# Kernel optimization log

Hardware: AMD Instinct MI355X
Metric: run time of the kernel (lower is better)

The kernel has to match this reference:

```python
import jax, jax.numpy as jnp
import numpy as np

N_NODES = 50000
N_EDGES = 800000
NODE_DIM = 27
HIDDEN = 64
CTX = 32
HEADS = 4
NEG_SLOPE = 0.2


def _gat_layer(x, src, dst, W, a_src, a_dst, bias, n_nodes):
    # x: [N, F_in], W: [F_in, H*C], a_src/a_dst: [H, C], bias: [C]
    h = (x @ W).reshape(n_nodes, HEADS, -1)            # [N, H, C]
    alpha_src = jnp.einsum('nhc,hc->nh', h, a_src)     # [N, H]
    alpha_dst = jnp.einsum('nhc,hc->nh', h, a_dst)     # [N, H]
    e = alpha_src[src] + alpha_dst[dst]                # [E, H]
    e = jax.nn.leaky_relu(e, NEG_SLOPE)
    # segment softmax over edges grouped by destination node
    e_max = jax.ops.segment_max(e, dst, num_segments=n_nodes)  # [N, H]
    e_exp = jnp.exp(e - e_max[dst])                    # [E, H]
    denom = jax.ops.segment_sum(e_exp, dst, num_segments=n_nodes)  # [N, H]
    alpha = e_exp / denom[dst]                         # [E, H]
    msg = alpha[:, :, None] * h[src]                   # [E, H, C]
    out = jax.ops.segment_sum(msg, dst, num_segments=n_nodes)      # [N, H, C]
    return out.mean(axis=1) + bias                     # concat=False -> head mean


def setup_inputs() -> dict:
    key = jax.random.key(0)
    ks = jax.random.split(key, 16)
    glorot = lambda k, shp: jax.random.normal(k, shp, jnp.float32) * jnp.sqrt(2.0 / (shp[0] + shp[-1]))
    inp = {
        'x': jax.random.normal(ks[0], (N_NODES, NODE_DIM), jnp.float32),
        'edge_index': jax.random.randint(ks[1], (2, N_EDGES), 0, N_NODES, jnp.int32),
        'donor_emb': jax.random.normal(ks[2], (1, CTX), jnp.float32),
        # GAT layer 1
        'W1': glorot(ks[3], (NODE_DIM, HEADS * HIDDEN)),
        'a_src1': glorot(ks[4], (HEADS, HIDDEN)),
        'a_dst1': glorot(ks[5], (HEADS, HIDDEN)),
        'b1': jnp.zeros((HIDDEN,), jnp.float32),
        # GAT layer 2
        'W2': glorot(ks[6], (HIDDEN, HEADS * HIDDEN)),
        'a_src2': glorot(ks[7], (HEADS, HIDDEN)),
        'a_dst2': glorot(ks[8], (HEADS, HIDDEN)),
        'b2': jnp.zeros((HIDDEN,), jnp.float32),
        # scorer MLP
        'Ws1': glorot(ks[9], (HIDDEN + CTX, HIDDEN)),
        'bs1': jnp.zeros((HIDDEN,), jnp.float32),
        'Ws2': glorot(ks[10], (HIDDEN, 1)),
        'bs2': jnp.zeros((1,), jnp.float32),
    }
    return inp


def reference(x, edge_index, donor_emb, W1, a_src1, a_dst1, b1,
              W2, a_src2, a_dst2, b2, Ws1, bs1, Ws2, bs2):
    n = x.shape[0]
    # PyG GATConv default add_self_loops=True
    loop = jnp.arange(n, dtype=edge_index.dtype)
    src = jnp.concatenate([edge_index[0], loop])
    dst = jnp.concatenate([edge_index[1], loop])

    h = jax.nn.elu(_gat_layer(x, src, dst, W1, a_src1, a_dst1, b1, n))
    h = jax.nn.elu(_gat_layer(h, src, dst, W2, a_src2, a_dst2, b2, n))

    ctx = jnp.concatenate([h, jnp.broadcast_to(donor_emb, (n, donor_emb.shape[-1]))], axis=-1)
    hidden = jax.nn.relu(ctx @ Ws1 + bs1)
    logits = (hidden @ Ws2 + bs2).squeeze(-1)          # [N]
    return logits
```

## Files before the change

### kernel.cpp

```cpp
#include <hip/hip_runtime.h>
#include <hip/hip_fp16.h>
#include <cmath>

#define NEG 0.2f

typedef __attribute__((ext_vector_type(8))) short short8;
typedef __attribute__((ext_vector_type(4))) float f32x4;
typedef __fp16 half2_t __attribute__((ext_vector_type(2)));

__device__ __forceinline__ float leaky(float v){ return v > 0.f ? v : NEG * v; }

__device__ __forceinline__ short bf16_rne(float f){
    unsigned u = __float_as_uint(f);
    unsigned r = u + 0x7fffu + ((u >> 16) & 1u);
    return (short)(r >> 16);
}
__device__ __forceinline__ float bf16_to_f(short s){
    return __uint_as_float(((unsigned)(unsigned short)s) << 16);
}
__device__ __forceinline__ half2_t bc16(unsigned u){ return __builtin_bit_cast(half2_t, u); }
__device__ __forceinline__ unsigned packh2(float a, float b){
    __half ha = __float2half(a), hb = __float2half(b);
    return (unsigned)__builtin_bit_cast(unsigned short, ha)
         | ((unsigned)__builtin_bit_cast(unsigned short, hb) << 16);
}

__device__ __forceinline__ int block_excl_scan(int v, int* ws4){
    int tid = threadIdx.x, lane = tid & 63, wv = tid >> 6;
    int incl = v;
    #pragma unroll
    for (int off = 1; off < 64; off <<= 1){
        int t = __shfl_up(incl, off);
        if (lane >= off) incl += t;
    }
    if (lane == 63) ws4[wv] = incl;
    __syncthreads();
    int add = 0;
    for (int w = 0; w < wv; ++w) add += ws4[w];
    return incl - v + add;
}


__global__ __launch_bounds__(256) void prep_hist_kernel(
    const float* __restrict__ W1, const float* __restrict__ W2,
    const float* __restrict__ Ws1, const float* __restrict__ bs1,
    const float* __restrict__ donor,
    const float* __restrict__ as1, const float* __restrict__ ad1,
    const float* __restrict__ as2, const float* __restrict__ ad2,
    short* __restrict__ w1p, short* __restrict__ w2p,
    short* __restrict__ s1hi, short* __restrict__ s1lo, float* __restrict__ d1p,
    float* __restrict__ hat1s, float* __restrict__ hat1d,
    float* __restrict__ hat2s, float* __restrict__ hat2d,
    const int* __restrict__ ei, int E, int N, int NB, int* __restrict__ bucket_cnt)
{
    if ((int)blockIdx.x < 256){
        int t = blockIdx.x * 256 + threadIdx.x;
        int T = 256 * 256;
        for (int i = t; i < 64 * 136; i += T){
            int c = i / 136, kk = i % 136; short v = 0;
            if (kk < 128){ int h = kk >> 5, k = kk & 31;
                if (k < 27) v = bf16_rne(W1[(size_t)k * 256 + h * 64 + c] * 0.25f); }
            w1p[i] = v;
        }
        for (int i = t; i < 64 * 264; i += T){
            int c = i / 264, kk = i % 264; short v = 0;
            if (kk < 256){ int h = kk >> 6, k = kk & 63;
                v = bf16_rne(W2[(size_t)k * 256 + h * 64 + c] * 0.25f); }
            w2p[i] = v;
        }
        for (int i = t; i < 64 * 72; i += T){
            int nn = i / 72, k = i % 72;
            float v = (k < 64) ? Ws1[(size_t)k * 64 + nn] : 0.f;
            short hi = bf16_rne(v);
            s1hi[i] = hi; s1lo[i] = bf16_rne(v - bf16_to_f(hi));
        }
        if (t < 64){
            float s = bs1[t];
            for (int k = 0; k < 32; ++k) s = fmaf(donor[k], Ws1[(size_t)(64 + k) * 64 + t], s);
            d1p[t] = s;
        }
        if (t < 128){
            int h = t >> 5, k = t & 31;
            float s = 0.f, d = 0.f;
            if (k < 27)
                for (int c = 0; c < 64; ++c){
                    float w = W1[(size_t)k * 256 + h * 64 + c];
                    s = fmaf(w, as1[h * 64 + c], s);
                    d = fmaf(w, ad1[h * 64 + c], d);
                }
            hat1s[t] = s; hat1d[t] = d;
        }
        if (t < 256){
            int h = t >> 6, k = t & 63;
            float s = 0.f, d = 0.f;
            for (int c = 0; c < 64; ++c){
                float w = W2[(size_t)k * 256 + h * 64 + c];
                s = fmaf(w, as2[h * 64 + c], s);
                d = fmaf(w, ad2[h * 64 + c], d);
            }
            hat2s[t] = s; hat2d[t] = d;
        }
    } else {
        __shared__ int lh[256];
        int tid = threadIdx.x;
        int ET = E + N;
        int ebase = ((int)blockIdx.x - 256) * 2048;
        lh[tid] = 0;
        __syncthreads();
        #pragma unroll
        for (int j = 0; j < 8; ++j){
            int e = ebase + j * 256 + tid;
            if (e < ET){
                int d = (e < E) ? ei[E + e] : (e - E);
                atomicAdd(&lh[d >> 8], 1);
            }
        }
        __syncthreads();
        if (tid < NB && lh[tid]) atomicAdd(&bucket_cnt[tid], lh[tid]);
    }
}


__global__ __launch_bounds__(256) void coarse_scatter_kernel(
    const int* __restrict__ ei, int E, int N, int NB,
    const int* __restrict__ bucket_cnt, int* __restrict__ bucket_cursor,
    unsigned* __restrict__ pairs)
{
    __shared__ int ws4[4];
    __shared__ int gbase[256];
    __shared__ int lh[256];
    __shared__ int gb[256];
    int tid = threadIdx.x;
    int ET = E + N;
    {
        int v = (tid < NB) ? bucket_cnt[tid] : 0;
        gbase[tid] = block_excl_scan(v, ws4);
    }
    lh[tid] = 0;
    __syncthreads();
    int ebase = blockIdx.x * 2048;
    int d[8], s[8], r[8];
    #pragma unroll
    for (int j = 0; j < 8; ++j){
        int e = ebase + j * 256 + tid;
        d[j] = -1;
        if (e < ET){
            if (e < E){ s[j] = ei[e]; d[j] = ei[E + e]; } else { s[j] = d[j] = e - E; }
            r[j] = atomicAdd(&lh[d[j] >> 8], 1);
        }
    }
    __syncthreads();
    if (tid < NB && lh[tid]) gb[tid] = gbase[tid] + atomicAdd(&bucket_cursor[tid], lh[tid]);
    __syncthreads();
    #pragma unroll
    for (int j = 0; j < 8; ++j){
        if (d[j] >= 0)
            pairs[gb[d[j] >> 8] + r[j]] = ((unsigned)d[j] << 16) | (unsigned)s[j];
    }
}


__device__ __forceinline__ void fine_sort_body(
    int b, const unsigned* __restrict__ pairs, const int* __restrict__ bucket_cnt, int NB,
    int* __restrict__ colsrc, int* __restrict__ rowptr, int N, int ET)
{
    __shared__ int ws4f[4];
    __shared__ int sb[257];
    __shared__ int hist[256];
    __shared__ int cur[256];
    int tid = threadIdx.x;
    {
        int v = (tid < NB) ? bucket_cnt[tid] : 0;
        int excl = block_excl_scan(v, ws4f);
        sb[tid] = excl;
        if (tid == 255) sb[256] = excl + v;
    }
    hist[tid] = 0;
    __syncthreads();
    int base = sb[b], endb = sb[b + 1];
    int cnt = endb - base;
    int d0 = b << 8;
    for (int i = tid; i < cnt; i += 256){
        unsigned p = pairs[base + i];
        atomicAdd(&hist[(int)(p >> 16) - d0], 1);
    }
    __syncthreads();
    int v = hist[tid];
    int excl = block_excl_scan(v, ws4f);
    cur[tid] = excl;
    if (d0 + tid < N) rowptr[d0 + tid] = base + excl;
    if (b == 0 && tid == 0) rowptr[N] = ET;
    __syncthreads();
    for (int i = tid; i < cnt; i += 256){
        unsigned p = pairs[base + i];
        int r = atomicAdd(&cur[(int)(p >> 16) - d0], 1);
        colsrc[base + r] = (int)(p & 0xFFFFu);
    }
}


__global__ __launch_bounds__(256) void xprep_fine_kernel(
    const float* __restrict__ x, const float* __restrict__ hat1s, const float* __restrict__ hat1d,
    float* __restrict__ xp, float* __restrict__ asrc, float* __restrict__ adst, int N,
    int XB, const unsigned* __restrict__ pairs, const int* __restrict__ bucket_cnt, int NB,
    int* __restrict__ colsrc, int* __restrict__ rowptr, int ET)
{
    if ((int)blockIdx.x < XB){
        int t0 = blockIdx.x * 256 + threadIdx.x, T = XB * 256;
        for (int i = t0; i < N * 32; i += T){
            int nn = i >> 5, k = i & 31;
            xp[i] = (k < 27) ? x[(size_t)nn * 27 + k] : 0.f;
        }
        for (int nn = t0; nn < N; nn += T){
            float xr[27];
            #pragma unroll
            for (int k = 0; k < 27; ++k) xr[k] = x[(size_t)nn * 27 + k];
            #pragma unroll
            for (int h = 0; h < 4; ++h){
                float s = 0.f, d = 0.f;
                #pragma unroll
                for (int k = 0; k < 27; ++k){
                    s = fmaf(xr[k], hat1s[h * 32 + k], s);
                    d = fmaf(xr[k], hat1d[h * 32 + k], d);
                }
                asrc[nn * 4 + h] = s;
                adst[nn * 4 + h] = d;
            }
        }
    } else {
        fine_sort_body(blockIdx.x - XB, pairs, bucket_cnt, NB, colsrc, rowptr, N, ET);
    }
}


template<int L>
__device__ __forceinline__ void agg_edge(const char* __restrict__ pay, int boff, int o,
    unsigned aw, unsigned bw, float* accx, float* accy)
{
    half2_t ah = bc16(aw), bh = bc16(bw);
    float w0 = (float)ah[0], w1 = (float)ah[1], w2 = (float)bh[0], w3 = (float)bh[1];
    if (L == 1){
        float xv = *(const float*)(pay + o + boff);
        accx[0] = fmaf(w0, xv, accx[0]);
        accx[1] = fmaf(w1, xv, accx[1]);
        accx[2] = fmaf(w2, xv, accx[2]);
        accx[3] = fmaf(w3, xv, accx[3]);
    } else {
        unsigned hv = *(const unsigned*)(pay + o + boff);
        half2_t hh = bc16(hv);
        float c0 = (float)hh[0], c1 = (float)hh[1];
        accx[0] = fmaf(w0, c0, accx[0]); accy[0] = fmaf(w0, c1, accy[0]);
        accx[1] = fmaf(w1, c0, accx[1]); accy[1] = fmaf(w1, c1, accy[1]);
        accx[2] = fmaf(w2, c0, accx[2]); accy[2] = fmaf(w2, c1, accy[2]);
        accx[3] = fmaf(w3, c0, accx[3]); accy[3] = fmaf(w3, c1, accy[3]);
    }
}

template<int L>
__global__ __launch_bounds__(256) void aggregate_kernel(
    const int* __restrict__ rowptr, const int* __restrict__ colsrc,
    const char* __restrict__ pay, const float* __restrict__ asrc,
    const float* __restrict__ adst, char* __restrict__ gout, int N)
{
    int tid = threadIdx.x;
    int grp = tid >> 5;
    int lane32 = tid & 31;
    int n = blockIdx.x * 8 + grp;
    if (n >= N) return;
    int start = rowptr[n], end = rowptr[n + 1];
    int deg = end - start;
    const float4 ad = *(const float4*)(adst + (size_t)n * 4);

    int src0 = 0;
    float e0 = -1e30f, e1 = -1e30f, e2 = -1e30f, e3 = -1e30f;
    bool v0 = lane32 < deg;
    if (v0){
        src0 = colsrc[start + lane32];
        float4 as = *(const float4*)(asrc + (size_t)src0 * 4);
        e0 = leaky(as.x + ad.x); e1 = leaky(as.y + ad.y);
        e2 = leaky(as.z + ad.z); e3 = leaky(as.w + ad.w);
    }

    float m0, m1, m2, m3, i0, i1, i2, i3, p0, p1, p2, p3;
    if (deg <= 32){
        m0 = e0; m1 = e1; m2 = e2; m3 = e3;
        #pragma unroll
        for (int off = 1; off < 32; off <<= 1){
            m0 = fmaxf(m0, __shfl_xor(m0, off));
            m1 = fmaxf(m1, __shfl_xor(m1, off));
            m2 = fmaxf(m2, __shfl_xor(m2, off));
            m3 = fmaxf(m3, __shfl_xor(m3, off));
        }
        p0 = __expf(e0 - m0);
        p1 = __expf(e1 - m1);
        p2 = __expf(e2 - m2);
        p3 = __expf(e3 - m3);
        float t0 = p0, t1 = p1, t2 = p2, t3 = p3;
        #pragma unroll
        for (int off = 1; off < 32; off <<= 1){
            t0 += __shfl_xor(t0, off);
            t1 += __shfl_xor(t1, off);
            t2 += __shfl_xor(t2, off);
            t3 += __shfl_xor(t3, off);
        }
        i0 = 1.f / t0; i1 = 1.f / t1; i2 = 1.f / t2; i3 = 1.f / t3;
    } else {
        m0 = e0; m1 = e1; m2 = e2; m3 = e3;
        float t0 = v0 ? 1.f : 0.f, t1 = t0, t2 = t0, t3 = t0;
        for (int i = start + 32 + lane32; i < end; i += 32){
            int s = colsrc[i];
            float4 as = *(const float4*)(asrc + (size_t)s * 4);
            float e, nm;
            e = leaky(as.x + ad.x); nm = fmaxf(m0, e); t0 = t0 * __expf(m0 - nm) + __expf(e - nm); m0 = nm;
            e = leaky(as.y + ad.y); nm = fmaxf(m1, e); t1 = t1 * __expf(m1 - nm) + __expf(e - nm); m1 = nm;
            e = leaky(as.z + ad.z); nm = fmaxf(m2, e); t2 = t2 * __expf(m2 - nm) + __expf(e - nm); m2 = nm;
            e = leaky(as.w + ad.w); nm = fmaxf(m3, e); t3 = t3 * __expf(m3 - nm) + __expf(e - nm); m3 = nm;
        }
        #pragma unroll
        for (int off = 1; off < 32; off <<= 1){
            float om, os, nm;
            om = __shfl_xor(m0, off); os = __shfl_xor(t0, off);
            nm = fmaxf(m0, om); t0 = t0 * __expf(m0 - nm) + os * __expf(om - nm); m0 = nm;
            om = __shfl_xor(m1, off); os = __shfl_xor(t1, off);
            nm = fmaxf(m1, om); t1 = t1 * __expf(m1 - nm) + os * __expf(om - nm); m1 = nm;
            om = __shfl_xor(m2, off); os = __shfl_xor(t2, off);
            nm = fmaxf(m2, om); t2 = t2 * __expf(m2 - nm) + os * __expf(om - nm); m2 = nm;
            om = __shfl_xor(m3, off); os = __shfl_xor(t3, off);
            nm = fmaxf(m3, om); t3 = t3 * __expf(m3 - nm) + os * __expf(om - nm); m3 = nm;
        }
        i0 = 1.f / t0; i1 = 1.f / t1; i2 = 1.f / t2; i3 = 1.f / t3;
        p0 = __expf(e0 - m0); p1 = __expf(e1 - m1);
        p2 = __expf(e2 - m2); p3 = __expf(e3 - m3);
    }

    float accx[4] = {0.f, 0.f, 0.f, 0.f};
    float accy[4] = {0.f, 0.f, 0.f, 0.f};
    const int boff = lane32 * 4;
    bool first = true;
    for (int base = start; base < end; base += 32){
        int cnt = end - base; if (cnt > 32) cnt = 32;
        float w0, w1, w2, w3; int off = 0;
        if (first){
            w0 = p0 * i0; w1 = p1 * i1; w2 = p2 * i2; w3 = p3 * i3;
            off = v0 ? src0 * 128 : 0;
        } else {
            w0 = w1 = w2 = w3 = 0.f;
            if (lane32 < cnt){
                int s = colsrc[base + lane32];
                float4 as = *(const float4*)(asrc + (size_t)s * 4);
                w0 = __expf(leaky(as.x + ad.x) - m0) * i0;
                w1 = __expf(leaky(as.y + ad.y) - m1) * i1;
                w2 = __expf(leaky(as.z + ad.z) - m2) * i2;
                w3 = __expf(leaky(as.w + ad.w) - m3) * i3;
                off = s * 128;
            }
        }
        first = false;
        half2_t q01 = __builtin_amdgcn_cvt_pkrtz(w0, w1);
        half2_t q23 = __builtin_amdgcn_cvt_pkrtz(w2, w3);
        int wx = (int)__builtin_bit_cast(unsigned, q01);
        int wy = (int)__builtin_bit_cast(unsigned, q23);

        int j = 0;
        for (; j + 2 <= cnt; j += 2){
            int o0 = __shfl(off, j, 32);
            unsigned a0 = (unsigned)__shfl(wx, j, 32), b0 = (unsigned)__shfl(wy, j, 32);
            int o1 = __shfl(off, j + 1, 32);
            unsigned a1 = (unsigned)__shfl(wx, j + 1, 32), b1 = (unsigned)__shfl(wy, j + 1, 32);
            agg_edge<L>(pay, boff, o0, a0, b0, accx, accy);
            agg_edge<L>(pay, boff, o1, a1, b1, accx, accy);
        }
        for (; j < cnt; ++j){
            int o0 = __shfl(off, j, 32);
            unsigned a0 = (unsigned)__shfl(wx, j, 32), b0 = (unsigned)__shfl(wy, j, 32);
            agg_edge<L>(pay, boff, o0, a0, b0, accx, accy);
        }
    }

    if (L == 1){
        float* g = (float*)gout;
        #pragma unroll
        for (int h = 0; h < 4; ++h)
            g[(size_t)n * 128 + h * 32 + lane32] = accx[h];
    } else {
        #pragma unroll
        for (int h = 0; h < 4; ++h){
            unsigned u = packh2(accx[h], accy[h]);
            *(unsigned*)(gout + (size_t)n * 512 + h * 128 + lane32 * 4) = u;
        }
    }
}


__global__ __launch_bounds__(256) void t1post_kernel(
    const float* __restrict__ G1, const short* __restrict__ w1p, const float* __restrict__ b1,
    const float* __restrict__ hat2s, const float* __restrict__ hat2d,
    __half* __restrict__ hm16, float* __restrict__ asrc, float* __restrict__ adst, int N)
{
    constexpr int WP = 136;
    __shared__ short wt[64 * WP];
    const int tid = threadIdx.x;
    const int n0 = blockIdx.x * 64;
    const int wv = tid >> 6, lane = tid & 63;
    const int quad = lane >> 4, ln = lane & 15;
    const int myrow = wv * 16 + ln;
    const int nme = n0 + myrow;

    {
        const short8* g = (const short8*)w1p;
        short8* l = (short8*)wt;
        for (int t = tid; t < 64 * WP / 8; t += 256) l[t] = g[t];
    }
    __syncthreads();

    f32x4 acc[4];
    #pragma unroll
    for (int i = 0; i < 4; ++i) acc[i] = (f32x4){0.f, 0.f, 0.f, 0.f};

    #pragma unroll
    for (int ks = 0; ks < 4; ++ks){
        const int k0 = ks * 32 + quad * 8;
        float4 f0 = make_float4(0.f, 0.f, 0.f, 0.f), f1 = f0;
        if (nme < N){
            const float* ap = G1 + (size_t)nme * 128 + k0;
            f0 = *(const float4*)ap;
            f1 = *(const float4*)(ap + 4);
        }
        float fa[8] = {f0.x, f0.y, f0.z, f0.w, f1.x, f1.y, f1.z, f1.w};
        short8 ahi, alo;
        #pragma unroll
        for (int e = 0; e < 8; ++e){
            short hi = bf16_rne(fa[e]);
            ahi[e] = hi;
            alo[e] = bf16_rne(fa[e] - bf16_to_f(hi));
        }
        #pragma unroll
        for (int nt = 0; nt < 4; ++nt){
            short8 bhi = *(const short8*)(wt + (nt * 16 + ln) * WP + k0);
            acc[nt] = __builtin_amdgcn_mfma_f32_16x16x32_bf16(ahi, bhi, acc[nt], 0, 0, 0);
            acc[nt] = __builtin_amdgcn_mfma_f32_16x16x32_bf16(alo, bhi, acc[nt], 0, 0, 0);
        }
    }

    float b1v[4], hs[4][4], hd[4][4];
    #pragma unroll
    for (int nt = 0; nt < 4; ++nt) b1v[nt] = b1[nt * 16 + ln];
    #pragma unroll
    for (int h = 0; h < 4; ++h)
        #pragma unroll
        for (int nt = 0; nt < 4; ++nt){
            hs[h][nt] = hat2s[h * 64 + nt * 16 + ln];
            hd[h][nt] = hat2d[h * 64 + nt * 16 + ln];
        }

    #pragma unroll
    for (int r = 0; r < 4; ++r){
        int n = n0 + wv * 16 + quad * 4 + r;
        float ev[4];
        #pragma unroll
        for (int nt = 0; nt < 4; ++nt){
            float v = acc[nt][r] + b1v[nt];
            v = (v > 0.f) ? v : expm1f(v);
            ev[nt] = v;
        }
        if (n < N){
            #pragma unroll
            for (int nt = 0; nt < 4; ++nt)
                hm16[(size_t)n * 64 + nt * 16 + ln] = __float2half(ev[nt]);
        }
        #pragma unroll
        for (int h = 0; h < 4; ++h){
            float ps = 0.f, pd = 0.f;
            #pragma unroll
            for (int nt = 0; nt < 4; ++nt){
                ps = fmaf(ev[nt], hs[h][nt], ps);
                pd = fmaf(ev[nt], hd[h][nt], pd);
            }
            #pragma unroll
            for (int off = 1; off < 16; off <<= 1){
                ps += __shfl_xor(ps, off);
                pd += __shfl_xor(pd, off);
            }
            if (ln == 0 && n < N){
                asrc[n * 4 + h] = ps;
                adst[n * 4 + h] = pd;
            }
        }
    }
}


__global__ __launch_bounds__(256) void t2post_kernel(
    const char* __restrict__ G2, const short* __restrict__ w2p, const float* __restrict__ b2,
    float* __restrict__ hmid2, int N)
{
    constexpr int WP = 264;
    __shared__ short wt[64 * WP];
    const int tid = threadIdx.x;
    const int n0 = blockIdx.x * 64;
    const int wv = tid >> 6, lane = tid & 63;
    const int quad = lane >> 4, ln = lane & 15;
    const int myrow = wv * 16 + ln;
    const int nme = n0 + myrow;

    {
        const short8* g = (const short8*)w2p;
        short8* l = (short8*)wt;
        for (int t = tid; t < 64 * WP / 8; t += 256) l[t] = g[t];
    }
    __syncthreads();

    f32x4 acc[4];
    #pragma unroll
    for (int i = 0; i < 4; ++i) acc[i] = (f32x4){0.f, 0.f, 0.f, 0.f};

    #pragma unroll
    for (int ks = 0; ks < 8; ++ks){
        const int k0 = ks * 32 + quad * 8;
        uint4 u = make_uint4(0u, 0u, 0u, 0u);
        if (nme < N)
            u = *(const uint4*)(G2 + (size_t)nme * 512 + (size_t)k0 * 2);
        half2_t h0 = bc16(u.x), h1 = bc16(u.y), h2 = bc16(u.z), h3 = bc16(u.w);
        float fa[8] = {(float)h0[0], (float)h0[1], (float)h1[0], (float)h1[1],
                       (float)h2[0], (float)h2[1], (float)h3[0], (float)h3[1]};
        short8 ahi, alo;
        #pragma unroll
        for (int e = 0; e < 8; ++e){
            short hi = bf16_rne(fa[e]);
            ahi[e] = hi;
            alo[e] = bf16_rne(fa[e] - bf16_to_f(hi));
        }
        #pragma unroll
        for (int nt = 0; nt < 4; ++nt){
            short8 bhi = *(const short8*)(wt + (nt * 16 + ln) * WP + k0);
            acc[nt] = __builtin_amdgcn_mfma_f32_16x16x32_bf16(ahi, bhi, acc[nt], 0, 0, 0);
            acc[nt] = __builtin_amdgcn_mfma_f32_16x16x32_bf16(alo, bhi, acc[nt], 0, 0, 0);
        }
    }

    float b2v[4];
    #pragma unroll
    for (int nt = 0; nt < 4; ++nt) b2v[nt] = b2[nt * 16 + ln];
    #pragma unroll
    for (int r = 0; r < 4; ++r){
        int n = n0 + wv * 16 + quad * 4 + r;
        if (n < N){
            #pragma unroll
            for (int nt = 0; nt < 4; ++nt){
                float v = acc[nt][r] + b2v[nt];
                v = (v > 0.f) ? v : expm1f(v);
                hmid2[(size_t)n * 64 + nt * 16 + ln] = v;
            }
        }
    }
}


__global__ __launch_bounds__(256) void scorer_mfma_kernel(
    const float* __restrict__ h2, const short* __restrict__ s1hi, const short* __restrict__ s1lo,
    const float* __restrict__ d1p, const float* __restrict__ Ws2, const float* __restrict__ bs2,
    float* __restrict__ out, int N)
{
    constexpr int WP = 72;
    __shared__ short whi[64 * WP];
    __shared__ short wlo[64 * WP];
    const int tid = threadIdx.x;
    const int n0 = blockIdx.x * 64;

    const int wv = tid >> 6, lane = tid & 63;
    const int quad = lane >> 4, ln = lane & 15;
    const int myrow = wv * 16 + ln;
    const int nme = n0 + myrow;

    float fdir[16];
    #pragma unroll
    for (int ks = 0; ks < 2; ++ks){
        float4 f0 = make_float4(0.f, 0.f, 0.f, 0.f), f1 = f0;
        if (nme < N){
            const float* ap = h2 + (size_t)nme * 64 + ks * 32 + quad * 8;
            f0 = *(const float4*)ap;
            f1 = *(const float4*)(ap + 4);
        }
        fdir[ks*8+0]=f0.x; fdir[ks*8+1]=f0.y; fdir[ks*8+2]=f0.z; fdir[ks*8+3]=f0.w;
        fdir[ks*8+4]=f1.x; fdir[ks*8+5]=f1.y; fdir[ks*8+6]=f1.z; fdir[ks*8+7]=f1.w;
    }
    {
        const short8* ghi = (const short8*)s1hi;
        const short8* glo = (const short8*)s1lo;
        short8* lhi = (short8*)whi;
        short8* llo = (short8*)wlo;
        for (int t = tid; t < 64 * WP / 8; t += 256){ lhi[t] = ghi[t]; llo[t] = glo[t]; }
    }
    __syncthreads();

    f32x4 acc[4];
    #pragma unroll
    for (int i = 0; i < 4; ++i) acc[i] = (f32x4){0.f, 0.f, 0.f, 0.f};

    #pragma unroll
    for (int ks = 0; ks < 2; ++ks) {
        const int k0 = ks * 32 + quad * 8;
        short8 ahi, alo;
        #pragma unroll
        for (int e = 0; e < 8; ++e) {
            float v = fdir[ks * 8 + e];
            short hi = bf16_rne(v);
            ahi[e] = hi;
            alo[e] = bf16_rne(v - bf16_to_f(hi));
        }
        #pragma unroll
        for (int nt = 0; nt < 4; ++nt) {
            short8 bhi = *(const short8*)(whi + (nt * 16 + ln) * WP + k0);
            short8 blo = *(const short8*)(wlo + (nt * 16 + ln) * WP + k0);
            acc[nt] = __builtin_amdgcn_mfma_f32_16x16x32_bf16(ahi, bhi, acc[nt], 0, 0, 0);
            acc[nt] = __builtin_amdgcn_mfma_f32_16x16x32_bf16(alo, bhi, acc[nt], 0, 0, 0);
            acc[nt] = __builtin_amdgcn_mfma_f32_16x16x32_bf16(ahi, blo, acc[nt], 0, 0, 0);
        }
    }

    float d1v[4], w2v[4];
    #pragma unroll
    for (int nt = 0; nt < 4; ++nt){
        d1v[nt] = d1p[nt * 16 + ln];
        w2v[nt] = Ws2[nt * 16 + ln];
    }
    float b2 = bs2[0];
    #pragma unroll
    for (int r = 0; r < 4; ++r){
        float t = 0.f;
        #pragma unroll
        for (int nt = 0; nt < 4; ++nt)
            t = fmaf(fmaxf(acc[nt][r] + d1v[nt], 0.f), w2v[nt], t);
        #pragma unroll
        for (int off = 1; off < 16; off <<= 1) t += __shfl_xor(t, off);
        if (ln == 0){
            int n = n0 + wv * 16 + quad * 4 + r;
            if (n < N) out[n] = t + b2;
        }
    }
}


extern "C" void kernel_launch(void* const* d_in, const int* in_sizes, int n_in,
                              void* d_out, int out_size, void* d_ws, size_t ws_size,
                              hipStream_t stream)
{
    const float* x    = (const float*)d_in[0];
    const int*   ei   = (const int*)  d_in[1];
    const float* donor= (const float*)d_in[2];
    const float* W1   = (const float*)d_in[3];
    const float* as1  = (const float*)d_in[4];
    const float* ad1  = (const float*)d_in[5];
    const float* b1   = (const float*)d_in[6];
    const float* W2   = (const float*)d_in[7];
    const float* as2  = (const float*)d_in[8];
    const float* ad2  = (const float*)d_in[9];
    const float* b2   = (const float*)d_in[10];
    const float* Ws1  = (const float*)d_in[11];
    const float* bs1  = (const float*)d_in[12];
    const float* Ws2  = (const float*)d_in[13];
    const float* bs2  = (const float*)d_in[14];

    const int N  = in_sizes[0] / 27;
    const int E  = in_sizes[1] / 2;
    const int ET = E + N;
    const int NB = (N + 255) / 256;

    char* ws = (char*)d_ws;
    auto alloc = [&](size_t bytes) -> void* {
        void* p = (void*)ws;
        ws += (bytes + 255) / 256 * 256;
        return p;
    };
    int*      rowptr  = (int*)     alloc((size_t)(N + 1) * 4);
    int*      colsrc  = (int*)     alloc((size_t)ET * 4);
    unsigned* pairs   = (unsigned*)alloc((size_t)ET * 4);
    float*    xp      = (float*)   alloc((size_t)N * 128);
    char*     gbuf    = (char*)    alloc((size_t)N * 512);
    __half*   hm16    = (__half*)  alloc((size_t)N * 128);
    float*    hmid2   = (float*)   alloc((size_t)N * 256);
    float*    asrc    = (float*)   alloc((size_t)N * 4 * 4);
    float*    adst    = (float*)   alloc((size_t)N * 4 * 4);
    int*      bucket_cnt    = (int*) alloc(256 * 4);
    int*      bucket_cursor = (int*) alloc(256 * 4);
    short*    w1p     = (short*)   alloc(64 * 136 * 2);
    short*    w2p     = (short*)   alloc(64 * 264 * 2);
    short*    s1hi    = (short*)   alloc(64 * 72 * 2);
    short*    s1lo    = (short*)   alloc(64 * 72 * 2);
    float*    d1p     = (float*)   alloc(64 * 4);
    float*    hat1s   = (float*)   alloc(128 * 4);
    float*    hat1d   = (float*)   alloc(128 * 4);
    float*    hat2s   = (float*)   alloc(256 * 4);
    float*    hat2d   = (float*)   alloc(256 * 4);

    const int nblk = (N + 63) / 64;
    const int hblk = (ET + 2047) / 2048;
    const int XB   = 512;

    (void)hipMemsetAsync(bucket_cnt, 0, 512 * 4, stream);
    prep_hist_kernel<<<256 + hblk, 256, 0, stream>>>(
        W1, W2, Ws1, bs1, donor, as1, ad1, as2, ad2,
        w1p, w2p, s1hi, s1lo, d1p, hat1s, hat1d, hat2s, hat2d,
        ei, E, N, NB, bucket_cnt);
    coarse_scatter_kernel<<<hblk, 256, 0, stream>>>(ei, E, N, NB, bucket_cnt, bucket_cursor, pairs);
    xprep_fine_kernel<<<XB + NB, 256, 0, stream>>>(
        x, hat1s, hat1d, xp, asrc, adst, N,
        XB, pairs, bucket_cnt, NB, colsrc, rowptr, ET);
    aggregate_kernel<1><<<(N + 7) / 8, 256, 0, stream>>>(
        rowptr, colsrc, (const char*)xp, asrc, adst, gbuf, N);
    t1post_kernel<<<nblk, 256, 0, stream>>>(
        (const float*)gbuf, w1p, b1, hat2s, hat2d, hm16, asrc, adst, N);
    aggregate_kernel<2><<<(N + 7) / 8, 256, 0, stream>>>(
        rowptr, colsrc, (const char*)hm16, asrc, adst, gbuf, N);
    t2post_kernel<<<nblk, 256, 0, stream>>>(
        (const char*)gbuf, w2p, b2, hmid2, N);
    scorer_mfma_kernel<<<nblk, 256, 0, stream>>>(
        hmid2, s1hi, s1lo, d1p, Ws2, bs2, (float*)d_out, N);
}
```

Before: 233.3 us.

## Fuse t2post with scorer, move x prep into prep kernel, store x as fp16

The t2post and scorer kernels become one kernel that keeps the layer-2 output in shared memory, so the fp32 hmid2 round trip through global memory and one launch go away. The x padding and layer-1 attention-logit computation move into the prep/histogram kernel, which now computes hat1 per block in shared memory. The fine sort becomes its own kernel. The padded x is stored as fp16, and layer-1 aggregation reads half2 with two edges per pass across half-warps, halving gather bytes at some cost in input precision.

```diff
diff --git a/kernel.cpp b/kernel.cpp
--- a/kernel.cpp
+++ b/kernel.cpp
@@ -47,14 +47,17 @@
     const float* __restrict__ donor,
     const float* __restrict__ as1, const float* __restrict__ ad1,
     const float* __restrict__ as2, const float* __restrict__ ad2,
+    const float* __restrict__ x,
     short* __restrict__ w1p, short* __restrict__ w2p,
     short* __restrict__ s1hi, short* __restrict__ s1lo, float* __restrict__ d1p,
-    float* __restrict__ hat1s, float* __restrict__ hat1d,
     float* __restrict__ hat2s, float* __restrict__ hat2d,
-    const int* __restrict__ ei, int E, int N, int NB, int* __restrict__ bucket_cnt)
+    __half* __restrict__ xp, float* __restrict__ asrc, float* __restrict__ adst,
+    const int* __restrict__ ei, int E, int N, int NB, int* __restrict__ bucket_cnt,
+    int hblk, int XBP)
 {
-    if ((int)blockIdx.x < 256){
-        int t = blockIdx.x * 256 + threadIdx.x;
+    int b = (int)blockIdx.x;
+    if (b < 256){
+        int t = b * 256 + threadIdx.x;
         int T = 256 * 256;
         for (int i = t; i < 64 * 136; i += T){
             int c = i / 136, kk = i % 136; short v = 0;
@@ -79,8 +82,38 @@
             for (int k = 0; k < 32; ++k) s = fmaf(donor[k], Ws1[(size_t)(64 + k) * 64 + t], s);
             d1p[t] = s;
         }
-        if (t < 128){
-            int h = t >> 5, k = t & 31;
+        if (t < 256){
+            int h = t >> 6, k = t & 63;
+            float s = 0.f, d = 0.f;
+            for (int c = 0; c < 64; ++c){
+                float w = W2[(size_t)k * 256 + h * 64 + c];
+                s = fmaf(w, as2[h * 64 + c], s);
+                d = fmaf(w, ad2[h * 64 + c], d);
+            }
+            hat2s[t] = s; hat2d[t] = d;
+        }
+    } else if (b < 256 + hblk){
+        __shared__ int lh[256];
+        int tid = threadIdx.x;
+        int ET = E + N;
+        int ebase = (b - 256) * 2048;
+        lh[tid] = 0;
+        __syncthreads();
+        #pragma unroll
+        for (int j = 0; j < 8; ++j){
+            int e = ebase + j * 256 + tid;
+            if (e < ET){
+                int d = (e < E) ? ei[E + e] : (e - E);
+                atomicAdd(&lh[d >> 8], 1);
+            }
+        }
+        __syncthreads();
+        if (tid < NB && lh[tid]) atomicAdd(&bucket_cnt[tid], lh[tid]);
+    } else {
+        __shared__ float h1s[128], h1d[128];
+        int tid = threadIdx.x;
+        if (tid < 128){
+            int h = tid >> 5, k = tid & 31;
             float s = 0.f, d = 0.f;
             if (k < 27)
                 for (int c = 0; c < 64; ++c){
@@ -88,35 +121,31 @@
                     s = fmaf(w, as1[h * 64 + c], s);
                     d = fmaf(w, ad1[h * 64 + c], d);
                 }
-            hat1s[t] = s; hat1d[t] = d;
-        }
-        if (t < 256){
-            int h = t >> 6, k = t & 63;
-            float s = 0.f, d = 0.f;
-            for (int c = 0; c < 64; ++c){
-                float w = W2[(size_t)k * 256 + h * 64 + c];
-                s = fmaf(w, as2[h * 64 + c], s);
-                d = fmaf(w, ad2[h * 64 + c], d);
-            }
-            hat2s[t] = s; hat2d[t] = d;
-        }
-    } else {
-        __shared__ int lh[256];
-        int tid = threadIdx.x;
-        int ET = E + N;
-        int ebase = ((int)blockIdx.x - 256) * 2048;
-        lh[tid] = 0;
+            h1s[tid] = s; h1d[tid] = d;
+        }
         __syncthreads();
-        #pragma unroll
-        for (int j = 0; j < 8; ++j){
-            int e = ebase + j * 256 + tid;
-            if (e < ET){
-                int d = (e < E) ? ei[E + e] : (e - E);
-                atomicAdd(&lh[d >> 8], 1);
-            }
-        }
-        __syncthreads();
-        if (tid < NB && lh[tid]) atomicAdd(&bucket_cnt[tid], lh[tid]);
+        int pb = b - 256 - hblk;
+        int t0 = pb * 256 + tid, T = XBP * 256;
+        for (int i = t0; i < N * 32; i += T){
+            int nn = i >> 5, k = i & 31;
+            xp[i] = __float2half((k < 27) ? x[(size_t)nn * 27 + k] : 0.f);
+        }
+        for (int nn = t0; nn < N; nn += T){
+            float xr[27];
+            #pragma unroll
+            for (int k = 0; k < 27; ++k) xr[k] = x[(size_t)nn * 27 + k];
+            #pragma unroll
+            for (int h = 0; h < 4; ++h){
+                float s = 0.f, d = 0.f;
+                #pragma unroll
+                for (int k = 0; k < 27; ++k){
+                    s = fmaf(xr[k], h1s[h * 32 + k], s);
+                    d = fmaf(xr[k], h1d[h * 32 + k], d);
+                }
+                asrc[nn * 4 + h] = s;
+                adst[nn * 4 + h] = d;
+            }
+        }
     }
 }
 
@@ -160,14 +189,15 @@
 }
 
 
-__device__ __forceinline__ void fine_sort_body(
-    int b, const unsigned* __restrict__ pairs, const int* __restrict__ bucket_cnt, int NB,
+__global__ __launch_bounds__(256) void fine_sort_kernel(
+    const unsigned* __restrict__ pairs, const int* __restrict__ bucket_cnt, int NB,
     int* __restrict__ colsrc, int* __restrict__ rowptr, int N, int ET)
 {
     __shared__ int ws4f[4];
     __shared__ int sb[257];
     __shared__ int hist[256];
     __shared__ int cur[256];
+    int b = (int)blockIdx.x;
     int tid = threadIdx.x;
     {
         int v = (tid < NB) ? bucket_cnt[tid] : 0;
@@ -199,69 +229,13 @@
 }
 
 
-__global__ __launch_bounds__(256) void xprep_fine_kernel(
-    const float* __restrict__ x, const float* __restrict__ hat1s, const float* __restrict__ hat1d,
-    float* __restrict__ xp, float* __restrict__ asrc, float* __restrict__ adst, int N,
-    int XB, const unsigned* __restrict__ pairs, const int* __restrict__ bucket_cnt, int NB,
-    int* __restrict__ colsrc, int* __restrict__ rowptr, int ET)
-{
-    if ((int)blockIdx.x < XB){
-        int t0 = blockIdx.x * 256 + threadIdx.x, T = XB * 256;
-        for (int i = t0; i < N * 32; i += T){
-            int nn = i >> 5, k = i & 31;
-            xp[i] = (k < 27) ? x[(size_t)nn * 27 + k] : 0.f;
-        }
-        for (int nn = t0; nn < N; nn += T){
-            float xr[27];
-            #pragma unroll
-            for (int k = 0; k < 27; ++k) xr[k] = x[(size_t)nn * 27 + k];
-            #pragma unroll
-            for (int h = 0; h < 4; ++h){
-                float s = 0.f, d = 0.f;
-                #pragma unroll
-                for (int k = 0; k < 27; ++k){
-                    s = fmaf(xr[k], hat1s[h * 32 + k], s);
-                    d = fmaf(xr[k], hat1d[h * 32 + k], d);
-                }
-                asrc[nn * 4 + h] = s;
-                adst[nn * 4 + h] = d;
-            }
-        }
-    } else {
-        fine_sort_body(blockIdx.x - XB, pairs, bucket_cnt, NB, colsrc, rowptr, N, ET);
-    }
-}
-
-
-template<int L>
-__device__ __forceinline__ void agg_edge(const char* __restrict__ pay, int boff, int o,
-    unsigned aw, unsigned bw, float* accx, float* accy)
-{
-    half2_t ah = bc16(aw), bh = bc16(bw);
-    float w0 = (float)ah[0], w1 = (float)ah[1], w2 = (float)bh[0], w3 = (float)bh[1];
-    if (L == 1){
-        float xv = *(const float*)(pay + o + boff);
-        accx[0] = fmaf(w0, xv, accx[0]);
-        accx[1] = fmaf(w1, xv, accx[1]);
-        accx[2] = fmaf(w2, xv, accx[2]);
-        accx[3] = fmaf(w3, xv, accx[3]);
-    } else {
-        unsigned hv = *(const unsigned*)(pay + o + boff);
-        half2_t hh = bc16(hv);
-        float c0 = (float)hh[0], c1 = (float)hh[1];
-        accx[0] = fmaf(w0, c0, accx[0]); accy[0] = fmaf(w0, c1, accy[0]);
-        accx[1] = fmaf(w1, c0, accx[1]); accy[1] = fmaf(w1, c1, accy[1]);
-        accx[2] = fmaf(w2, c0, accx[2]); accy[2] = fmaf(w2, c1, accy[2]);
-        accx[3] = fmaf(w3, c0, accx[3]); accy[3] = fmaf(w3, c1, accy[3]);
-    }
-}
-
 template<int L>
 __global__ __launch_bounds__(256) void aggregate_kernel(
     const int* __restrict__ rowptr, const int* __restrict__ colsrc,
     const char* __restrict__ pay, const float* __restrict__ asrc,
     const float* __restrict__ adst, char* __restrict__ gout, int N)
 {
+    constexpr int RS = (L == 1) ? 64 : 128;
     int tid = threadIdx.x;
     int grp = tid >> 5;
     int lane32 = tid & 31;
@@ -335,14 +309,15 @@
 
     float accx[4] = {0.f, 0.f, 0.f, 0.f};
     float accy[4] = {0.f, 0.f, 0.f, 0.f};
-    const int boff = lane32 * 4;
+    const int half = lane32 >> 4;
+    const int boff = (L == 1) ? (lane32 & 15) * 4 : lane32 * 4;
     bool first = true;
     for (int base = start; base < end; base += 32){
         int cnt = end - base; if (cnt > 32) cnt = 32;
         float w0, w1, w2, w3; int off = 0;
         if (first){
             w0 = p0 * i0; w1 = p1 * i1; w2 = p2 * i2; w3 = p3 * i3;
-            off = v0 ? src0 * 128 : 0;
+            off = v0 ? src0 * RS : 0;
         } else {
             w0 = w1 = w2 = w3 = 0.f;
             if (lane32 < cnt){
@@ -352,7 +327,7 @@
                 w1 = __expf(leaky(as.y + ad.y) - m1) * i1;
                 w2 = __expf(leaky(as.z + ad.z) - m2) * i2;
                 w3 = __expf(leaky(as.w + ad.w) - m3) * i3;
-                off = s * 128;
+                off = s * RS;
             }
         }
         first = false;
@@ -361,27 +336,55 @@
         int wx = (int)__builtin_bit_cast(unsigned, q01);
         int wy = (int)__builtin_bit_cast(unsigned, q23);
 
-        int j = 0;
-        for (; j + 2 <= cnt; j += 2){
-            int o0 = __shfl(off, j, 32);
-            unsigned a0 = (unsigned)__shfl(wx, j, 32), b0 = (unsigned)__shfl(wy, j, 32);
-            int o1 = __shfl(off, j + 1, 32);
-            unsigned a1 = (unsigned)__shfl(wx, j + 1, 32), b1 = (unsigned)__shfl(wy, j + 1, 32);
-            agg_edge<L>(pay, boff, o0, a0, b0, accx, accy);
-            agg_edge<L>(pay, boff, o1, a1, b1, accx, accy);
-        }
-        for (; j < cnt; ++j){
-            int o0 = __shfl(off, j, 32);
-            unsigned a0 = (unsigned)__shfl(wx, j, 32), b0 = (unsigned)__shfl(wy, j, 32);
-            agg_edge<L>(pay, boff, o0, a0, b0, accx, accy);
+        if (L == 1){
+            for (int j = 0; j < cnt; j += 2){
+                int jj = j + half;
+                int sel = (jj < cnt) ? jj : 0;
+                int o = __shfl(off, sel, 32);
+                unsigned aw = (unsigned)__shfl(wx, sel, 32);
+                unsigned bw = (unsigned)__shfl(wy, sel, 32);
+                if (jj >= cnt){ aw = 0u; bw = 0u; }
+                unsigned xv = *(const unsigned*)(pay + o + boff);
+                half2_t xh = bc16(xv);
+                float c0 = (float)xh[0], c1 = (float)xh[1];
+                half2_t ah = bc16(aw), bh = bc16(bw);
+                float f0 = (float)ah[0], f1 = (float)ah[1], f2 = (float)bh[0], f3 = (float)bh[1];
+                accx[0] = fmaf(f0, c0, accx[0]); accy[0] = fmaf(f0, c1, accy[0]);
+                accx[1] = fmaf(f1, c0, accx[1]); accy[1] = fmaf(f1, c1, accy[1]);
+                accx[2] = fmaf(f2, c0, accx[2]); accy[2] = fmaf(f2, c1, accy[2]);
+                accx[3] = fmaf(f3, c0, accx[3]); accy[3] = fmaf(f3, c1, accy[3]);
+            }
+        } else {
+            for (int j = 0; j < cnt; ++j){
+                int o = __shfl(off, j, 32);
+                unsigned aw = (unsigned)__shfl(wx, j, 32);
+                unsigned bw = (unsigned)__shfl(wy, j, 32);
+                unsigned hv = *(const unsigned*)(pay + o + boff);
+                half2_t hh = bc16(hv);
+                float c0 = (float)hh[0], c1 = (float)hh[1];
+                half2_t ah = bc16(aw), bh = bc16(bw);
+                float f0 = (float)ah[0], f1 = (float)ah[1], f2 = (float)bh[0], f3 = (float)bh[1];
+                accx[0] = fmaf(f0, c0, accx[0]); accy[0] = fmaf(f0, c1, accy[0]);
+                accx[1] = fmaf(f1, c0, accx[1]); accy[1] = fmaf(f1, c1, accy[1]);
+                accx[2] = fmaf(f2, c0, accx[2]); accy[2] = fmaf(f2, c1, accy[2]);
+                accx[3] = fmaf(f3, c0, accx[3]); accy[3] = fmaf(f3, c1, accy[3]);
+            }
         }
     }
 
     if (L == 1){
-        float* g = (float*)gout;
-        #pragma unroll
-        for (int h = 0; h < 4; ++h)
-            g[(size_t)n * 128 + h * 32 + lane32] = accx[h];
+        #pragma unroll
+        for (int h = 0; h < 4; ++h){
+            accx[h] += __shfl_xor(accx[h], 16);
+            accy[h] += __shfl_xor(accy[h], 16);
+        }
+        if (lane32 < 16){
+            float* g = (float*)gout;
+            #pragma unroll
+            for (int h = 0; h < 4; ++h)
+                *(float2*)(g + (size_t)n * 128 + h * 32 + 2 * lane32) =
+                    make_float2(accx[h], accy[h]);
+        }
     } else {
         #pragma unroll
         for (int h = 0; h < 4; ++h){
@@ -490,12 +493,15 @@
 }
 
 
-__global__ __launch_bounds__(256) void t2post_kernel(
+__global__ __launch_bounds__(256) void t2post_scorer_kernel(
     const char* __restrict__ G2, const short* __restrict__ w2p, const float* __restrict__ b2,
-    float* __restrict__ hmid2, int N)
+    const short* __restrict__ s1hi, const short* __restrict__ s1lo,
+    const float* __restrict__ d1p, const float* __restrict__ Ws2, const float* __restrict__ bs2,
+    float* __restrict__ out, int N)
 {
-    constexpr int WP = 264;
-    __shared__ short wt[64 * WP];
+    constexpr int WP2 = 264;
+    constexpr int WPS = 72;
+    __shared__ __align__(16) char S[64 * 68 * 4 + 2 * 64 * WPS * 2];
     const int tid = threadIdx.x;
     const int n0 = blockIdx.x * 64;
     const int wv = tid >> 6, lane = tid & 63;
@@ -503,10 +509,11 @@
     const int myrow = wv * 16 + ln;
     const int nme = n0 + myrow;
 
+    short* wt = (short*)S;
     {
         const short8* g = (const short8*)w2p;
         short8* l = (short8*)wt;
-        for (int t = tid; t < 64 * WP / 8; t += 256) l[t] = g[t];
+        for (int t = tid; t < 64 * WP2 / 8; t += 256) l[t] = g[t];
     }
     __syncthreads();
 
@@ -532,7 +539,7 @@
         }
         #pragma unroll
         for (int nt = 0; nt < 4; ++nt){
-            short8 bhi = *(const short8*)(wt + (nt * 16 + ln) * WP + k0);
+            short8 bhi = *(const short8*)(wt + (nt * 16 + ln) * WP2 + k0);
             acc[nt] = __builtin_amdgcn_mfma_f32_16x16x32_bf16(ahi, bhi, acc[nt], 0, 0, 0);
             acc[nt] = __builtin_amdgcn_mfma_f32_16x16x32_bf16(alo, bhi, acc[nt], 0, 0, 0);
         }
@@ -541,80 +548,53 @@
     float b2v[4];
     #pragma unroll
     for (int nt = 0; nt < 4; ++nt) b2v[nt] = b2[nt * 16 + ln];
+
+    __syncthreads();
+    float* hm  = (float*)S;
+    short* whi = (short*)(S + 64 * 68 * 4);
+    short* wlo = whi + 64 * WPS;
+
     #pragma unroll
     for (int r = 0; r < 4; ++r){
-        int n = n0 + wv * 16 + quad * 4 + r;
-        if (n < N){
-            #pragma unroll
-            for (int nt = 0; nt < 4; ++nt){
-                float v = acc[nt][r] + b2v[nt];
-                v = (v > 0.f) ? v : expm1f(v);
-                hmid2[(size_t)n * 64 + nt * 16 + ln] = v;
-            }
-        }
-    }
-}
-
-
-__global__ __launch_bounds__(256) void scorer_mfma_kernel(
-    const float* __restrict__ h2, const short* __restrict__ s1hi, const short* __restrict__ s1lo,
-    const float* __restrict__ d1p, const float* __restrict__ Ws2, const float* __restrict__ bs2,
-    float* __restrict__ out, int N)
-{
-    constexpr int WP = 72;
-    __shared__ short whi[64 * WP];
-    __shared__ short wlo[64 * WP];
-    const int tid = threadIdx.x;
-    const int n0 = blockIdx.x * 64;
-
-    const int wv = tid >> 6, lane = tid & 63;
-    const int quad = lane >> 4, ln = lane & 15;
-    const int myrow = wv * 16 + ln;
-    const int nme = n0 + myrow;
-
-    float fdir[16];
-    #pragma unroll
-    for (int ks = 0; ks < 2; ++ks){
-        float4 f0 = make_float4(0.f, 0.f, 0.f, 0.f), f1 = f0;
-        if (nme < N){
-            const float* ap = h2 + (size_t)nme * 64 + ks * 32 + quad * 8;
-            f0 = *(const float4*)ap;
-            f1 = *(const float4*)(ap + 4);
-        }
-        fdir[ks*8+0]=f0.x; fdir[ks*8+1]=f0.y; fdir[ks*8+2]=f0.z; fdir[ks*8+3]=f0.w;
-        fdir[ks*8+4]=f1.x; fdir[ks*8+5]=f1.y; fdir[ks*8+6]=f1.z; fdir[ks*8+7]=f1.w;
+        int row = wv * 16 + quad * 4 + r;
+        #pragma unroll
+        for (int nt = 0; nt < 4; ++nt){
+            float v = acc[nt][r] + b2v[nt];
+            v = (v > 0.f) ? v : expm1f(v);
+            hm[row * 68 + nt * 16 + ln] = v;
+        }
     }
     {
         const short8* ghi = (const short8*)s1hi;
         const short8* glo = (const short8*)s1lo;
         short8* lhi = (short8*)whi;
         short8* llo = (short8*)wlo;
-        for (int t = tid; t < 64 * WP / 8; t += 256){ lhi[t] = ghi[t]; llo[t] = glo[t]; }
-    }
-    __syncthreads();
-
-    f32x4 acc[4];
-    #pragma unroll
-    for (int i = 0; i < 4; ++i) acc[i] = (f32x4){0.f, 0.f, 0.f, 0.f};
-
-    #pragma unroll
-    for (int ks = 0; ks < 2; ++ks) {
+        for (int t = tid; t < 64 * WPS / 8; t += 256){ lhi[t] = ghi[t]; llo[t] = glo[t]; }
+    }
+    __syncthreads();
+
+    f32x4 acc2[4];
+    #pragma unroll
+    for (int i = 0; i < 4; ++i) acc2[i] = (f32x4){0.f, 0.f, 0.f, 0.f};
+
+    #pragma unroll
+    for (int ks = 0; ks < 2; ++ks){
         const int k0 = ks * 32 + quad * 8;
         short8 ahi, alo;
         #pragma unroll
-        for (int e = 0; e < 8; ++e) {
-            float v = fdir[ks * 8 + e];
+        for (int e = 0; e < 8; ++e){
+            float v = hm[myrow * 68 + k0 + e];
             short hi = bf16_rne(v);
             ahi[e] = hi;
             alo[e] = bf16_rne(v - bf16_to_f(hi));
         }
         #pragma unroll
-        for (int nt = 0; nt < 4; ++nt) {
-            short8 bhi = *(const short8*)(whi + (nt * 16 + ln) * WP + k0);
-            short8 blo = *(const short8*)(wlo + (nt * 16 + ln) * WP + k0);
-            acc[nt] = __builtin_amdgcn_mfma_f32_16x16x32_bf16(ahi, bhi, acc[nt], 0, 0, 0);
-            acc[nt] = __builtin_amdgcn_mfma_f32_16x16x32_bf16(alo, bhi, acc[nt], 0, 0, 0);
-            acc[nt] = __builtin_amdgcn_mfma_f32_16x16x32_bf16(ahi, blo, acc[nt], 0, 0, 0);
+        for (int nt = 0; nt < 4; ++nt){
+            short8 bhi = *(const short8*)(whi + (nt * 16 + ln) * WPS + k0);
+            short8 blo = *(const short8*)(wlo + (nt * 16 + ln) * WPS + k0);
+            acc2[nt] = __builtin_amdgcn_mfma_f32_16x16x32_bf16(ahi, bhi, acc2[nt], 0, 0, 0);
+            acc2[nt] = __builtin_amdgcn_mfma_f32_16x16x32_bf16(alo, bhi, acc2[nt], 0, 0, 0);
+            acc2[nt] = __builtin_amdgcn_mfma_f32_16x16x32_bf16(ahi, blo, acc2[nt], 0, 0, 0);
         }
     }
 
@@ -624,18 +604,18 @@
         d1v[nt] = d1p[nt * 16 + ln];
         w2v[nt] = Ws2[nt * 16 + ln];
     }
-    float b2 = bs2[0];
+    float bsv = bs2[0];
     #pragma unroll
     for (int r = 0; r < 4; ++r){
         float t = 0.f;
         #pragma unroll
         for (int nt = 0; nt < 4; ++nt)
-            t = fmaf(fmaxf(acc[nt][r] + d1v[nt], 0.f), w2v[nt], t);
+            t = fmaf(fmaxf(acc2[nt][r] + d1v[nt], 0.f), w2v[nt], t);
         #pragma unroll
         for (int off = 1; off < 16; off <<= 1) t += __shfl_xor(t, off);
         if (ln == 0){
             int n = n0 + wv * 16 + quad * 4 + r;
-            if (n < N) out[n] = t + b2;
+            if (n < N) out[n] = t + bsv;
         }
     }
 }
@@ -675,10 +655,9 @@
     int*      rowptr  = (int*)     alloc((size_t)(N + 1) * 4);
     int*      colsrc  = (int*)     alloc((size_t)ET * 4);
     unsigned* pairs   = (unsigned*)alloc((size_t)ET * 4);
-    float*    xp      = (float*)   alloc((size_t)N * 128);
+    __half*   xp      = (__half*)  alloc((size_t)N * 64);
     char*     gbuf    = (char*)    alloc((size_t)N * 512);
     __half*   hm16    = (__half*)  alloc((size_t)N * 128);
-    float*    hmid2   = (float*)   alloc((size_t)N * 256);
     float*    asrc    = (float*)   alloc((size_t)N * 4 * 4);
     float*    adst    = (float*)   alloc((size_t)N * 4 * 4);
     int*      bucket_cnt    = (int*) alloc(256 * 4);
@@ -688,32 +667,26 @@
     short*    s1hi    = (short*)   alloc(64 * 72 * 2);
     short*    s1lo    = (short*)   alloc(64 * 72 * 2);
     float*    d1p     = (float*)   alloc(64 * 4);
-    float*    hat1s   = (float*)   alloc(128 * 4);
-    float*    hat1d   = (float*)   alloc(128 * 4);
     float*    hat2s   = (float*)   alloc(256 * 4);
     float*    hat2d   = (float*)   alloc(256 * 4);
 
     const int nblk = (N + 63) / 64;
     const int hblk = (ET + 2047) / 2048;
-    const int XB   = 512;
+    const int XBP  = 512;
 
     (void)hipMemsetAsync(bucket_cnt, 0, 512 * 4, stream);
-    prep_hist_kernel<<<256 + hblk, 256, 0, stream>>>(
-        W1, W2, Ws1, bs1, donor, as1, ad1, as2, ad2,
-        w1p, w2p, s1hi, s1lo, d1p, hat1s, hat1d, hat2s, hat2d,
-        ei, E, N, NB, bucket_cnt);
+    prep_hist_kernel<<<256 + hblk + XBP, 256, 0, stream>>>(
+        W1, W2, Ws1, bs1, donor, as1, ad1, as2, ad2, x,
+        w1p, w2p, s1hi, s1lo, d1p, hat2s, hat2d,
+        xp, asrc, adst, ei, E, N, NB, bucket_cnt, hblk, XBP);
     coarse_scatter_kernel<<<hblk, 256, 0, stream>>>(ei, E, N, NB, bucket_cnt, bucket_cursor, pairs);
-    xprep_fine_kernel<<<XB + NB, 256, 0, stream>>>(
-        x, hat1s, hat1d, xp, asrc, adst, N,
-        XB, pairs, bucket_cnt, NB, colsrc, rowptr, ET);
+    fine_sort_kernel<<<NB, 256, 0, stream>>>(pairs, bucket_cnt, NB, colsrc, rowptr, N, ET);
     aggregate_kernel<1><<<(N + 7) / 8, 256, 0, stream>>>(
         rowptr, colsrc, (const char*)xp, asrc, adst, gbuf, N);
     t1post_kernel<<<nblk, 256, 0, stream>>>(
         (const float*)gbuf, w1p, b1, hat2s, hat2d, hm16, asrc, adst, N);
     aggregate_kernel<2><<<(N + 7) / 8, 256, 0, stream>>>(
         rowptr, colsrc, (const char*)hm16, asrc, adst, gbuf, N);
-    t2post_kernel<<<nblk, 256, 0, stream>>>(
-        (const char*)gbuf, w2p, b2, hmid2, N);
-    scorer_mfma_kernel<<<nblk, 256, 0, stream>>>(
-        hmid2, s1hi, s1lo, d1p, Ws2, bs2, (float*)d_out, N);
-}
+    t2post_scorer_kernel<<<nblk, 256, 0, stream>>>(
+        gbuf, w2p, b2, s1hi, s1lo, d1p, Ws2, bs2, (float*)d_out, N);
+}
```

Result: slower. 241.4 us (+3.5%).
